# Kernel tuning notes

Measured on AMD Instinct MI355X. Metric: run time of the kernel, lower is better.

The kernel has to match this reference:

```python
import jax, jax.numpy as jnp
import numpy as np

B, L, D, NC, H = 2, 192, 768, 4, 256  # batch, seq_len, bert_hidden, num_case(+coref), hidden


def setup_inputs() -> dict:
    key = jax.random.key(0)
    ks = jax.random.split(key, 9)
    s = 0.02  # init scale
    return {
        "sequence_output": jax.random.normal(ks[0], (B, L, D), dtype=jnp.float32),
        "base_score": jax.random.normal(ks[1], (B, L, NC, L), dtype=jnp.float32),
        "Wp": jax.random.normal(ks[2], (D, H), dtype=jnp.float32) * s,
        "bp": jnp.zeros((H,), dtype=jnp.float32),
        "Wa": jax.random.normal(ks[3], (D, NC * H), dtype=jnp.float32) * s,
        "ba": jnp.zeros((NC * H,), dtype=jnp.float32),
        "Wmid": jax.random.normal(ks[4], (NC, H + NC, H), dtype=jnp.float32) * s,
        "bmid": jnp.zeros((NC, H), dtype=jnp.float32),
        "Wout": jax.random.normal(ks[5], (NC, H), dtype=jnp.float32) * s,
    }


def reference(sequence_output, base_score, Wp, bp, Wa, ba, Wmid, bmid, Wout):
    b, l, d = sequence_output.shape
    nc = Wmid.shape[0]
    h = Wp.shape[1]
    # dropout is identity in eval mode
    h_p = sequence_output @ Wp + bp                       # [B, L, H] (predicate)
    h_a = (sequence_output @ Wa + ba).reshape(b, l, nc, h)  # [B, L, NC, H] (argument)
    # broadcast add: predicate axis p, argument axis a -> [B, P, A, NC, H]
    h_pa = jnp.tanh(h_p[:, :, None, None, :] + h_a[:, None, :, :, :])
    # base_score [B, L, NC, L] -> transpose(2,3) -> [B, P, A, NC], expand over case axis
    bs = jnp.swapaxes(base_score, 2, 3)                   # [B, P, A, NC]
    bs = jnp.broadcast_to(bs[:, :, :, None, :], (b, l, l, nc, nc))
    hcat = jnp.concatenate([h_pa, bs], axis=-1)           # [B, P, A, NC, H+NC]
    # per-case mid Linear, batched as a single einsum over the case axis n
    h_mid = jnp.tanh(jnp.einsum('bpanc,nch->bpanh', hcat, Wmid) + bmid)
    out = jnp.einsum('bpanh,nh->bpan', h_mid, Wout)       # [B, P, A, NC]
    return jnp.transpose(out, (0, 1, 3, 2))               # [B, P, NC, A]
```

## Files before the change

### kernel.cpp

```cpp
#include <hip/hip_runtime.h>

#define LSEQ 192
#define DIM  768
#define NCASE 4
#define HID  256
#define BATCH 2

#define TANH_K 2.885390081777927f

typedef float  floatx4 __attribute__((ext_vector_type(4)));
typedef __bf16 bf16x8  __attribute__((ext_vector_type(8)));

__device__ __forceinline__ float tanh_pre(float x) {
    float e = __builtin_amdgcn_exp2f(x);
    return 1.0f - 2.0f * __builtin_amdgcn_rcpf(e + 1.0f);
}

template <int CTRL>
__device__ __forceinline__ float dpp_add(float v) {
    int x = __builtin_amdgcn_update_dpp(0, __builtin_bit_cast(int, v),
                                        CTRL, 0xF, 0xF, true);
    return v + __builtin_bit_cast(float, x);
}
__device__ __forceinline__ float row16_reduce(float v) {
    v = dpp_add<0xB1>(v);
    v = dpp_add<0x4E>(v);
    v = dpp_add<0x141>(v);
    v = dpp_add<0x140>(v);
    return v;
}


__global__ __launch_bounds__(256) void pack_all(
    const float* __restrict__ seq, const float* __restrict__ Wp,
    const float* __restrict__ Wa, const float* __restrict__ Wmid,
    const float* __restrict__ bmid,
    bf16x8* __restrict__ seq_hi, bf16x8* __restrict__ seq_lo,
    bf16x8* __restrict__ W_hi,   bf16x8* __restrict__ W_lo,
    bf16x8* __restrict__ Bpack)
{
    int t = blockIdx.x * 256 + threadIdx.x;
    if (t < 36864) {
        const float* s = seq + (size_t)t * 8;
        bf16x8 hi, lo;
        #pragma unroll
        for (int j = 0; j < 8; j++) {
            float v = s[j];
            __bf16 h = (__bf16)v;
            hi[j] = h;
            lo[j] = (__bf16)(v - (float)h);
        }
        seq_hi[t] = hi; seq_lo[t] = lo;
    } else if (t < 159744) {
        int u = t - 36864;
        int lane = u & 63, f = u >> 6;
        int ctg = f % 80, kc = f / 80;
        int col16 = lane & 15, quad = lane >> 4;
        int col = ctg * 16 + col16;
        bf16x8 hi, lo;
        #pragma unroll
        for (int j = 0; j < 8; j++) {
            int k = kc * 32 + quad * 8 + j;
            float v = (col < 256) ? Wp[(size_t)k * HID + col]
                                  : Wa[(size_t)k * (NCASE * HID) + col - 256];
            __bf16 h = (__bf16)v;
            hi[j] = h;
            lo[j] = (__bf16)(v - (float)h);
        }
        W_hi[u] = hi; W_lo[u] = lo;
    } else {
        int u = t - 159744;
        int lane = u & 63, f = u >> 6;
        int ct = f & 15, nk = f >> 4;
        int kc = nk % 9, n = nk / 9;
        int col16 = lane & 15, quad = lane >> 4;
        int h = ct * 16 + col16;
        bf16x8 v;
        #pragma unroll
        for (int j = 0; j < 8; j++) {
            int k = kc * 32 + quad * 8 + j;
            float x;
            if (k < 260)       x = Wmid[(size_t)(n * 260 + k) * 256 + h];
            else if (k == 260) x = bmid[n * 256 + h];
            else               x = 0.0f;
            v[j] = (__bf16)(TANH_K * x);
        }
        Bpack[u] = v;
    }
}

__global__ __launch_bounds__(64) void lin_mfma(
    const bf16x8* __restrict__ seq_hi, const bf16x8* __restrict__ seq_lo,
    const bf16x8* __restrict__ W_hi,   const bf16x8* __restrict__ W_lo,
    const float* __restrict__ bp, const float* __restrict__ ba,
    float* __restrict__ lin)
{
    const int rt = blockIdx.x;
    const int cg = blockIdx.y;
    const int lane  = threadIdx.x;
    const int quad  = lane >> 4;
    const int col16 = lane & 15;

    const int abase = (rt * 16 + col16) * 96 + quad;
    const int bbase = cg * 64 + lane;
    floatx4 acc = {};

    bf16x8 ah = seq_hi[abase], al = seq_lo[abase];
    bf16x8 bh = W_hi[bbase],   bl = W_lo[bbase];
    #pragma unroll
    for (int kc = 0; kc < 24; kc++) {
        bf16x8 ah2, al2, bh2, bl2;
        if (kc < 23) {
            ah2 = seq_hi[abase + (kc + 1) * 4];
            al2 = seq_lo[abase + (kc + 1) * 4];
            bh2 = W_hi[bbase + (kc + 1) * 5120];
            bl2 = W_lo[bbase + (kc + 1) * 5120];
        }
        acc = __builtin_amdgcn_mfma_f32_16x16x32_bf16(ah, bh, acc, 0, 0, 0);
        acc = __builtin_amdgcn_mfma_f32_16x16x32_bf16(al, bh, acc, 0, 0, 0);
        acc = __builtin_amdgcn_mfma_f32_16x16x32_bf16(ah, bl, acc, 0, 0, 0);
        ah = ah2; al = al2; bh = bh2; bl = bl2;
    }
    const int col = cg * 16 + col16;
    const float bias = (col < 256) ? bp[col] : ba[col - 256];
    #pragma unroll
    for (int reg = 0; reg < 4; reg++)
        lin[(size_t)(rt * 16 + quad * 4 + reg) * 1280 + col] =
            TANH_K * (acc[reg] + bias);
}

__global__ __launch_bounds__(256, 2) void refine_main(
    const float* __restrict__ lin,
    const float* __restrict__ base_score,
    const float* __restrict__ Wout,
    const bf16x8* __restrict__ Bpack,
    float* __restrict__ out)
{
    const int bx = blockIdx.x;
    const int n  = blockIdx.y;
    const int b  = blockIdx.z;
    const int ptile = bx / 24, atile = bx % 24;
    const int p0 = ptile * 8, a0 = atile * 8;

    const int tid   = threadIdx.x;
    const int w     = tid >> 6;
    const int lane  = tid & 63;
    const int quad  = lane >> 4;
    const int col16 = lane & 15;

    __shared__ __align__(16) __bf16 A0[256 * 8];
    __shared__ __align__(16) __bf16 A1[256 * 8];
    __shared__ float red[4][64];

    const int row_gen = w * 16 + col16;
    const int pg = p0 + (row_gen >> 3), ag = a0 + (row_gen & 7);
    const float* hp_ptr = lin + (size_t)(b * LSEQ + pg) * 1280 + quad * 8;
    const float* ha_ptr = lin + (size_t)(b * LSEQ + ag) * 1280 + 256 + n * 256 + quad * 8;

    const bf16x8* bbase = Bpack + ((size_t)(n * 9) * 16 + w * 4) * 64 + lane;

    float bs4[4], wo[4];
    #pragma unroll
    for (int j = 0; j < 4; j++)
        bs4[j] = base_score[((size_t)(b * LSEQ + pg) * NCASE + j) * LSEQ + ag];
    #pragma unroll
    for (int ct = 0; ct < 4; ct++)
        wo[ct] = Wout[n * 256 + w * 64 + ct * 16 + col16];

    bf16x8 bcur[4];
    #pragma unroll
    for (int ct = 0; ct < 4; ct++) bcur[ct] = bbase[ct * 64];

    floatx4 hp0 = *(const floatx4*)(hp_ptr);
    floatx4 hp1 = *(const floatx4*)(hp_ptr + 4);
    floatx4 ha0 = *(const floatx4*)(ha_ptr);
    floatx4 ha1 = *(const floatx4*)(ha_ptr + 4);
    {
        floatx4 s0 = hp0 + ha0, s1 = hp1 + ha1;
        bf16x8 av;
        #pragma unroll
        for (int j = 0; j < 4; j++) {
            av[j]     = (__bf16)tanh_pre(s0[j]);
            av[4 + j] = (__bf16)tanh_pre(s1[j]);
        }
        *(bf16x8*)&A0[tid * 8] = av;
    }
    hp0 = *(const floatx4*)(hp_ptr + 32);
    hp1 = *(const floatx4*)(hp_ptr + 36);
    ha0 = *(const floatx4*)(ha_ptr + 32);
    ha1 = *(const floatx4*)(ha_ptr + 36);
    __syncthreads();

    floatx4 acc[4][4] = {};

    #pragma unroll
    for (int kc = 0; kc < 9; kc++) {
        bf16x8 bnext[4];
        if (kc < 8) {
            #pragma unroll
            for (int ct = 0; ct < 4; ct++)
                bnext[ct] = bbase[((kc + 1) * 16 + ct) * 64];
        }
        if (kc < 7) {
            floatx4 s0 = hp0 + ha0, s1 = hp1 + ha1;
            if (kc < 6) {
                hp0 = *(const floatx4*)(hp_ptr + (kc + 2) * 32);
                hp1 = *(const floatx4*)(hp_ptr + (kc + 2) * 32 + 4);
                ha0 = *(const floatx4*)(ha_ptr + (kc + 2) * 32);
                ha1 = *(const floatx4*)(ha_ptr + (kc + 2) * 32 + 4);
            }
            bf16x8 av;
            #pragma unroll
            for (int j = 0; j < 4; j++) {
                av[j]     = (__bf16)tanh_pre(s0[j]);
                av[4 + j] = (__bf16)tanh_pre(s1[j]);
            }
            __bf16* buf = ((kc + 1) & 1) ? A1 : A0;
            *(bf16x8*)&buf[tid * 8] = av;
        } else if (kc == 7) {
            bf16x8 av = {};
            if (quad == 0) {
                #pragma unroll
                for (int j = 0; j < 4; j++) av[j] = (__bf16)bs4[j];
                av[4] = (__bf16)1.0f;
            }
            *(bf16x8*)&A0[tid * 8] = av;
        }

        const __bf16* rb = (kc & 1) ? A1 : A0;
        bf16x8 af[4];
        #pragma unroll
        for (int rt = 0; rt < 4; rt++)
            af[rt] = *(const bf16x8*)&rb[(rt * 64 + lane) * 8];
        #pragma unroll
        for (int rt = 0; rt < 4; rt++)
            #pragma unroll
            for (int ct = 0; ct < 4; ct++)
                acc[rt][ct] = __builtin_amdgcn_mfma_f32_16x16x32_bf16(
                    af[rt], bcur[ct], acc[rt][ct], 0, 0, 0);
        #pragma unroll
        for (int ct = 0; ct < 4; ct++) bcur[ct] = bnext[ct];
        if (kc < 8) __syncthreads();
    }

    #pragma unroll
    for (int rt = 0; rt < 4; rt++) {
        #pragma unroll
        for (int reg = 0; reg < 4; reg++) {
            float rs = 0.0f;
            #pragma unroll
            for (int ct = 0; ct < 4; ct++)
                rs += tanh_pre(acc[rt][ct][reg]) * wo[ct];
            rs = row16_reduce(rs);
            if (col16 == 0) red[w][rt * 16 + quad * 4 + reg] = rs;
        }
    }
    __syncthreads();

    if (tid < 64) {
        float total = red[0][tid] + red[1][tid] + red[2][tid] + red[3][tid];
        const int p = p0 + (tid >> 3), a = a0 + (tid & 7);
        out[((size_t)(b * LSEQ + p) * NCASE + n) * LSEQ + a] = total;
    }
}

extern "C" void kernel_launch(void* const* d_in, const int* in_sizes, int n_in,
                              void* d_out, int out_size, void* d_ws, size_t ws_size,
                              hipStream_t stream) {
    const float* seq  = (const float*)d_in[0];
    const float* bsc  = (const float*)d_in[1];
    const float* Wp   = (const float*)d_in[2];
    const float* bp   = (const float*)d_in[3];
    const float* Wa   = (const float*)d_in[4];
    const float* ba   = (const float*)d_in[5];
    const float* Wmid = (const float*)d_in[6];
    const float* bmid = (const float*)d_in[7];
    const float* Wout = (const float*)d_in[8];
    float* out = (float*)d_out;

    char* ws = (char*)d_ws;
    bf16x8* seq_hi = (bf16x8*)(ws);
    bf16x8* seq_lo = (bf16x8*)(ws +  589824);
    bf16x8* W_hi   = (bf16x8*)(ws + 1179648);
    bf16x8* W_lo   = (bf16x8*)(ws + 3145728);
    bf16x8* Bpack  = (bf16x8*)(ws + 5111808);
    float*  lin    = (float*) (ws + 5701632);

    pack_all<<<768, 256, 0, stream>>>(seq, Wp, Wa, Wmid, bmid,
                                      seq_hi, seq_lo, W_hi, W_lo, Bpack);
    lin_mfma<<<dim3(24, 80), 64, 0, stream>>>(seq_hi, seq_lo, W_hi, W_lo,
                                              bp, ba, lin);
    refine_main<<<dim3(576, NCASE, BATCH), 256, 0, stream>>>(
        lin, bsc, Wout, Bpack, out);
}
```

Baseline: 166.2 us.

## Fuse packing into linear MFMA kernel and use LDS-only barriers

Merges the bf16 hi/lo packing pass and the linear projection kernel into one prep kernel that converts fp32 inputs to split bf16 in registers just before each MFMA. A second set of blocks in the same launch builds the Wmid pack. This drops one kernel launch and the workspace round trip for the packed sequence and weights. The cost is redundant conversion work and strided, uncoalesced fp32 weight loads. Separately, __syncthreads in refine_main is replaced by a barrier that waits only on LDS counters (waitcnt 0xC07F), so outstanding global prefetches need not drain before the barrier.

```diff
diff --git a/kernel.cpp b/kernel.cpp
--- a/kernel.cpp
+++ b/kernel.cpp
@@ -14,6 +14,13 @@
 __device__ __forceinline__ float tanh_pre(float x) {
     float e = __builtin_amdgcn_exp2f(x);
     return 1.0f - 2.0f * __builtin_amdgcn_rcpf(e + 1.0f);
+}
+
+__device__ __forceinline__ void barrier_lds_only() {
+    __builtin_amdgcn_sched_barrier(0);
+    __builtin_amdgcn_s_waitcnt(0xC07F);
+    __builtin_amdgcn_s_barrier();
+    __builtin_amdgcn_sched_barrier(0);
 }
 
 template <int CTRL>
@@ -31,54 +38,27 @@
 }
 
 
-__global__ __launch_bounds__(256) void pack_all(
+__global__ __launch_bounds__(256) void prep(
     const float* __restrict__ seq, const float* __restrict__ Wp,
-    const float* __restrict__ Wa, const float* __restrict__ Wmid,
+    const float* __restrict__ Wa,  const float* __restrict__ bp,
+    const float* __restrict__ ba,  const float* __restrict__ Wmid,
     const float* __restrict__ bmid,
-    bf16x8* __restrict__ seq_hi, bf16x8* __restrict__ seq_lo,
-    bf16x8* __restrict__ W_hi,   bf16x8* __restrict__ W_lo,
-    bf16x8* __restrict__ Bpack)
+    float* __restrict__ lin, bf16x8* __restrict__ Bpack)
 {
-    int t = blockIdx.x * 256 + threadIdx.x;
-    if (t < 36864) {
-        const float* s = seq + (size_t)t * 8;
-        bf16x8 hi, lo;
-        #pragma unroll
-        for (int j = 0; j < 8; j++) {
-            float v = s[j];
-            __bf16 h = (__bf16)v;
-            hi[j] = h;
-            lo[j] = (__bf16)(v - (float)h);
-        }
-        seq_hi[t] = hi; seq_lo[t] = lo;
-    } else if (t < 159744) {
-        int u = t - 36864;
-        int lane = u & 63, f = u >> 6;
-        int ctg = f % 80, kc = f / 80;
-        int col16 = lane & 15, quad = lane >> 4;
-        int col = ctg * 16 + col16;
-        bf16x8 hi, lo;
-        #pragma unroll
-        for (int j = 0; j < 8; j++) {
-            int k = kc * 32 + quad * 8 + j;
-            float v = (col < 256) ? Wp[(size_t)k * HID + col]
-                                  : Wa[(size_t)k * (NCASE * HID) + col - 256];
-            __bf16 h = (__bf16)v;
-            hi[j] = h;
-            lo[j] = (__bf16)(v - (float)h);
-        }
-        W_hi[u] = hi; W_lo[u] = lo;
-    } else {
-        int u = t - 159744;
+    const int blk = blockIdx.x;
+    const int tid = threadIdx.x;
+
+    if (blk >= 480) {
+        int u = (blk - 480) * 256 + tid;
         int lane = u & 63, f = u >> 6;
         int ct = f & 15, nk = f >> 4;
         int kc = nk % 9, n = nk / 9;
-        int col16 = lane & 15, quad = lane >> 4;
-        int h = ct * 16 + col16;
+        int h = ct * 16 + (lane & 15);
+        int kbase = kc * 32 + ((lane >> 4) & 3) * 8;
         bf16x8 v;
         #pragma unroll
         for (int j = 0; j < 8; j++) {
-            int k = kc * 32 + quad * 8 + j;
+            int k = kbase + j;
             float x;
             if (k < 260)       x = Wmid[(size_t)(n * 260 + k) * 256 + h];
             else if (k == 260) x = bmid[n * 256 + h];
@@ -86,43 +66,55 @@
             v[j] = (__bf16)(TANH_K * x);
         }
         Bpack[u] = v;
-    }
-}
-
-__global__ __launch_bounds__(64) void lin_mfma(
-    const bf16x8* __restrict__ seq_hi, const bf16x8* __restrict__ seq_lo,
-    const bf16x8* __restrict__ W_hi,   const bf16x8* __restrict__ W_lo,
-    const float* __restrict__ bp, const float* __restrict__ ba,
-    float* __restrict__ lin)
-{
-    const int rt = blockIdx.x;
-    const int cg = blockIdx.y;
-    const int lane  = threadIdx.x;
+        return;
+    }
+
+    const int w = tid >> 6, lane = tid & 63;
+    const int u = blk * 4 + w;
+    const int rt = u / 80, cg = u % 80;
     const int quad  = lane >> 4;
     const int col16 = lane & 15;
 
-    const int abase = (rt * 16 + col16) * 96 + quad;
-    const int bbase = cg * 64 + lane;
+    const int arow = rt * 16 + col16;
+    const int col  = cg * 16 + col16;
+    const float* aptr = seq + (size_t)arow * DIM + quad * 8;
+    const float* wbase = (cg < 16) ? (Wp + col) : (Wa + (col - 256));
+    const int    wstr  = (cg < 16) ? HID : (NCASE * HID);
+
     floatx4 acc = {};
-
-    bf16x8 ah = seq_hi[abase], al = seq_lo[abase];
-    bf16x8 bh = W_hi[bbase],   bl = W_lo[bbase];
+    floatx4 a0 = *(const floatx4*)(aptr);
+    floatx4 a1 = *(const floatx4*)(aptr + 4);
+    float bv[8];
+    #pragma unroll
+    for (int j = 0; j < 8; j++) bv[j] = wbase[(size_t)(quad * 8 + j) * wstr];
+
     #pragma unroll
     for (int kc = 0; kc < 24; kc++) {
-        bf16x8 ah2, al2, bh2, bl2;
+        bf16x8 ah, al, bh, bl;
+        #pragma unroll
+        for (int j = 0; j < 4; j++) {
+            __bf16 h0 = (__bf16)a0[j];
+            ah[j] = h0; al[j] = (__bf16)(a0[j] - (float)h0);
+            __bf16 h1 = (__bf16)a1[j];
+            ah[4 + j] = h1; al[4 + j] = (__bf16)(a1[j] - (float)h1);
+        }
+        #pragma unroll
+        for (int j = 0; j < 8; j++) {
+            __bf16 h = (__bf16)bv[j];
+            bh[j] = h; bl[j] = (__bf16)(bv[j] - (float)h);
+        }
         if (kc < 23) {
-            ah2 = seq_hi[abase + (kc + 1) * 4];
-            al2 = seq_lo[abase + (kc + 1) * 4];
-            bh2 = W_hi[bbase + (kc + 1) * 5120];
-            bl2 = W_lo[bbase + (kc + 1) * 5120];
+            a0 = *(const floatx4*)(aptr + (kc + 1) * 32);
+            a1 = *(const floatx4*)(aptr + (kc + 1) * 32 + 4);
+            #pragma unroll
+            for (int j = 0; j < 8; j++)
+                bv[j] = wbase[(size_t)((kc + 1) * 32 + quad * 8 + j) * wstr];
         }
         acc = __builtin_amdgcn_mfma_f32_16x16x32_bf16(ah, bh, acc, 0, 0, 0);
         acc = __builtin_amdgcn_mfma_f32_16x16x32_bf16(al, bh, acc, 0, 0, 0);
         acc = __builtin_amdgcn_mfma_f32_16x16x32_bf16(ah, bl, acc, 0, 0, 0);
-        ah = ah2; al = al2; bh = bh2; bl = bl2;
-    }
-    const int col = cg * 16 + col16;
-    const float bias = (col < 256) ? bp[col] : ba[col - 256];
+    }
+    const float bias = (cg < 16) ? bp[col] : ba[col - 256];
     #pragma unroll
     for (int reg = 0; reg < 4; reg++)
         lin[(size_t)(rt * 16 + quad * 4 + reg) * 1280 + col] =
@@ -189,7 +181,7 @@
     hp1 = *(const floatx4*)(hp_ptr + 36);
     ha0 = *(const floatx4*)(ha_ptr + 32);
     ha1 = *(const floatx4*)(ha_ptr + 36);
-    __syncthreads();
+    barrier_lds_only();
 
     floatx4 acc[4][4] = {};
 
@@ -240,7 +232,7 @@
                     af[rt], bcur[ct], acc[rt][ct], 0, 0, 0);
         #pragma unroll
         for (int ct = 0; ct < 4; ct++) bcur[ct] = bnext[ct];
-        if (kc < 8) __syncthreads();
+        if (kc < 8) barrier_lds_only();
     }
 
     #pragma unroll
@@ -255,7 +247,7 @@
             if (col16 == 0) red[w][rt * 16 + quad * 4 + reg] = rs;
         }
     }
-    __syncthreads();
+    barrier_lds_only();
 
     if (tid < 64) {
         float total = red[0][tid] + red[1][tid] + red[2][tid] + red[3][tid];
@@ -279,17 +271,10 @@
     float* out = (float*)d_out;
 
     char* ws = (char*)d_ws;
-    bf16x8* seq_hi = (bf16x8*)(ws);
-    bf16x8* seq_lo = (bf16x8*)(ws +  589824);
-    bf16x8* W_hi   = (bf16x8*)(ws + 1179648);
-    bf16x8* W_lo   = (bf16x8*)(ws + 3145728);
-    bf16x8* Bpack  = (bf16x8*)(ws + 5111808);
-    float*  lin    = (float*) (ws + 5701632);
-
-    pack_all<<<768, 256, 0, stream>>>(seq, Wp, Wa, Wmid, bmid,
-                                      seq_hi, seq_lo, W_hi, W_lo, Bpack);
-    lin_mfma<<<dim3(24, 80), 64, 0, stream>>>(seq_hi, seq_lo, W_hi, W_lo,
-                                              bp, ba, lin);
+    float*  lin   = (float*)(ws);
+    bf16x8* Bpack = (bf16x8*)(ws + 1966080);
+
+    prep<<<624, 256, 0, stream>>>(seq, Wp, Wa, bp, ba, Wmid, bmid, lin, Bpack);
     refine_main<<<dim3(576, NCASE, BATCH), 256, 0, stream>>>(
         lin, bsc, Wout, Bpack, out);
 }
```

Measured after the change: 151.8 us. -8.7%, faster.
